# Kernel tuning notes

Measured on AMD Instinct MI355X. Metric: run time of the kernel, lower is better.

## Reference

```python
import jax, jax.numpy as jnp
import numpy as np

CAPACITY = 65536
HIDDEN = 512
NUM_HASHES = 8
HASH_SIZE = 16
BATCH = 2048


def setup_inputs() -> dict:
    key = jax.random.key(0)
    ks = jax.random.split(key, 6)
    scale = 1.0 / np.sqrt(HIDDEN)
    query = jax.random.normal(ks[0], (BATCH, HIDDEN), dtype=jnp.float32)
    memory_keys = jax.random.normal(ks[1], (CAPACITY, HIDDEN), dtype=jnp.float32) * scale
    memory_values = jax.random.normal(ks[2], (CAPACITY, HIDDEN), dtype=jnp.float32) * scale
    hash_projections = jax.random.normal(ks[3], (NUM_HASHES, HIDDEN, HASH_SIZE), dtype=jnp.float32) * scale
    out_w = jax.random.normal(ks[4], (HIDDEN, HIDDEN), dtype=jnp.float32) * scale  # torch Linear weight [out,in]
    out_b = jnp.zeros((HIDDEN,), dtype=jnp.float32)
    return {"query": query, "memory_keys": memory_keys, "memory_values": memory_values,
            "hash_projections": hash_projections, "out_w": out_w, "out_b": out_b, "top_k": 32}


def _compute_hash(x, hash_projections):
    # x: [m, h] -> hash bits [m, num_hashes] in {0,1}
    # einsum 'bh,nhd->bnd' then sum over d then sign-threshold
    proj = jnp.einsum('mh,nhd->mnd', x, hash_projections)
    return (proj.sum(-1) > 0).astype(jnp.int32)


def reference(query, memory_keys, memory_values, hash_projections, out_w, out_b, top_k):
    b, h = query.shape
    q_hash = _compute_hash(query, hash_projections)                    # [b, n]
    k_hash = _compute_hash(memory_keys, hash_projections)              # [c, n] (no_grad in torch)
    # Hamming distance via +/-1 dot product: dot = n - 2*dist (avoids [b,c,n] bool tensor)
    qf = (q_hash * 2 - 1).astype(jnp.float32)
    kf = (k_hash * 2 - 1).astype(jnp.float32)
    dot = jnp.einsum('bn,cn->bc', qf, kf)                              # [b, c]
    hash_dist = ((NUM_HASHES - dot) * 0.5).astype(jnp.int32)           # [b, c]
    k = min(top_k, memory_keys.shape[0])
    _, top_indices = jax.lax.top_k(-hash_dist, k)                      # smallest distances, [b, k]
    selected_keys = memory_keys[top_indices]                           # [b, k, h]
    selected_values = memory_values[top_indices]                       # [b, k, h]
    scores = jnp.einsum('bh,bkh->bk', query, selected_keys) / np.sqrt(h).astype(np.float32)
    attn = jax.nn.softmax(scores, axis=-1)
    memory_output = jnp.einsum('bk,bkh->bh', attn, selected_values)    # [b, h]
    return memory_output @ out_w.T + out_b
```

## Files before the change

kernel.cpp:

```cpp
#include <hip/hip_runtime.h>
#include <stdint.h>

#define BATCH  2048
#define HID    512
#define CAP    65536
#define NHASH  8
#define TOPK   32
#define NSLICE 16
#define SLICE_SZ (CAP / NSLICE)
#define ROWS_TILE 16
#define QTILES (BATCH / ROWS_TILE)
#define KTILES (CAP / ROWS_TILE)
#define TOT_TILES (QTILES + KTILES)
#define HGRID  768

typedef unsigned int   u32;
typedef unsigned long long u64;
typedef double d4 __attribute__((ext_vector_type(4)));

__global__ __launch_bounds__(256) void k_prep(const float* __restrict__ proj,
                                              double* __restrict__ psumT,
                                              u32* __restrict__ hist16,
                                              const float* __restrict__ w,
                                              float* __restrict__ wt) {
    __shared__ float tile[64][65];
    int bi = blockIdx.x, tid = threadIdx.x;
    if (bi < 2) {
        int g = bi * 256 + tid;
        for (int i = g; i < NSLICE * 256; i += 512) hist16[i] = 0;
        int h = g;
        for (int n = 0; n < NHASH; n++) {
            const float* p = proj + ((size_t)n * HID + h) * 16;
            double s = 0.0;
            #pragma unroll
            for (int d = 0; d < 16; d++) s += (double)p[d];
            psumT[(size_t)h * NHASH + n] = s;
        }
    } else {
        int b = bi - 2, bx = b & 7, by = b >> 3;
        int tx = tid & 63, ty = tid >> 6;
        for (int r = ty; r < 64; r += 4)
            tile[r][tx] = w[(size_t)(by * 64 + r) * HID + bx * 64 + tx];
        __syncthreads();
        for (int r = ty; r < 64; r += 4)
            wt[(size_t)(bx * 64 + r) * HID + by * 64 + tx] = tile[tx][r];
    }
}

__global__ __launch_bounds__(256, 3) void k_hash(const float* __restrict__ query,
                                                 const float* __restrict__ keys,
                                                 const double* __restrict__ psumT,
                                                 unsigned char* __restrict__ qhash,
                                                 unsigned char* __restrict__ khash,
                                                 u32* __restrict__ hist16) {
    __shared__ __align__(16) float sX[ROWS_TILE * HID];
    __shared__ double sAcc4[4][ROWS_TILE][8];

    const int tid  = threadIdx.x;
    const int w    = tid >> 6;
    const int m    = (tid & 63) & 15;
    const int kk   = (tid & 63) >> 4;

    d4 z = {0.0, 0.0, 0.0, 0.0};
    d4 pr = __builtin_amdgcn_mfma_f64_16x16x4f64((double)(m + 1), 1.0, z, 0, 0, 0);
    d4 pc = __builtin_amdgcn_mfma_f64_16x16x4f64(1.0, (double)(m + 1), z, 0, 0, 0);
    d4 pp = __builtin_amdgcn_mfma_f64_16x16x4f64((double)(1 << kk),
                                                 (double)(1 << (4 * kk)), z, 0, 0, 0);
    int rowOf[4], colOf[4];
    #pragma unroll
    for (int i = 0; i < 4; i++) {
        rowOf[i] = (int)(pr[i] * 0.25) - 1;
        colOf[i] = (int)(pc[i] * 0.25) - 1;
    }
    u32 pb = (u32)pp[0];
    u32 pairPacked = 0;
    #pragma unroll
    for (int e = 0; e < 16; e++)
        if ((pb >> e) & 1u) pairPacked |= (u32)(e & 3) << (2 * (e >> 2));

    const int kAdj = (int)((pairPacked >> (2 * kk)) & 3u);
    double bfrag[32];
    #pragma unroll
    for (int j = 0; j < 32; j++) {
        int kp = 128 * w + 4 * j + kAdj;
        bfrag[j] = (m < 8) ? psumT[(size_t)kp * NHASH + m] : 0.0;
    }

    const int sw = (m & 7) << 2;

    float4 pf[8];

    {
        int tt = blockIdx.x;
        const float* xb = (tt < QTILES)
            ? (query + (size_t)tt * ROWS_TILE * HID)
            : (keys + (size_t)(tt - QTILES) * ROWS_TILE * HID);
        #pragma unroll
        for (int p = 0; p < 8; p++) {
            int i = tid + 256 * p, r = i >> 7, G = i & 127;
            pf[p] = ((const float4*)(xb + (size_t)r * HID))[G];
        }
        #pragma unroll
        for (int p = 0; p < 8; p++) {
            int i = tid + 256 * p, r = i >> 7, G = i & 127;
            ((float4*)sX)[r * 128 + (G ^ (r & 7))] = pf[p];
        }
        __syncthreads();
    }

    int tt = blockIdx.x;
    for (;;) {
        const int tn = tt + HGRID;
        const bool more = (tn < TOT_TILES);

        if (more) {
            const float* xb = (tn < QTILES)
                ? (query + (size_t)tn * ROWS_TILE * HID)
                : (keys + (size_t)(tn - QTILES) * ROWS_TILE * HID);
            #pragma unroll
            for (int p = 0; p < 8; p++) {
                int i = tid + 256 * p, r = i >> 7, G = i & 127;
                pf[p] = ((const float4*)(xb + (size_t)r * HID))[G];
            }
        }

        d4 ac0 = z, ac1 = z, ac2 = z, ac3 = z;
        const float* sxm = sX + m * HID;
        #pragma unroll
        for (int j8 = 0; j8 < 8; j8++) {
            int k0 = 128 * w + ((4 * j8) ^ sw) + kk;
            ac0 = __builtin_amdgcn_mfma_f64_16x16x4f64((double)sxm[k0],      bfrag[j8],      ac0, 0, 0, 0);
            ac1 = __builtin_amdgcn_mfma_f64_16x16x4f64((double)sxm[k0 + 32], bfrag[j8 + 8],  ac1, 0, 0, 0);
            ac2 = __builtin_amdgcn_mfma_f64_16x16x4f64((double)sxm[k0 + 64], bfrag[j8 + 16], ac2, 0, 0, 0);
            ac3 = __builtin_amdgcn_mfma_f64_16x16x4f64((double)sxm[k0 + 96], bfrag[j8 + 24], ac3, 0, 0, 0);
        }
        d4 acc = (ac0 + ac1) + (ac2 + ac3);

        #pragma unroll
        for (int i = 0; i < 4; i++) {
            if (((unsigned)rowOf[i] < (unsigned)ROWS_TILE) && ((unsigned)colOf[i] < 8u))
                sAcc4[w][rowOf[i]][colOf[i]] = acc[i];
        }
        __syncthreads();

        if (tid < ROWS_TILE) {
            u32 byte = 0;
            #pragma unroll
            for (int n = 0; n < 8; n++) {
                double s = sAcc4[0][tid][n] + sAcc4[1][tid][n]
                         + sAcc4[2][tid][n] + sAcc4[3][tid][n];
                if (s > 0.0) byte |= (1u << n);
            }
            if (tt < QTILES) {
                qhash[tt * ROWS_TILE + tid] = (unsigned char)byte;
            } else {
                int row = (tt - QTILES) * ROWS_TILE + tid;
                khash[row] = (unsigned char)byte;
                atomicAdd(&hist16[(row / SLICE_SZ) * 256 + byte], 1u);
            }
        }
        if (!more) break;

        #pragma unroll
        for (int p = 0; p < 8; p++) {
            int i = tid + 256 * p, r = i >> 7, G = i & 127;
            ((float4*)sX)[r * 128 + (G ^ (r & 7))] = pf[p];
        }
        __syncthreads();
        tt = tn;
    }
}

__global__ __launch_bounds__(256) void k_scan(const u32* __restrict__ hist16,
                                              u32* __restrict__ bucketCnt,
                                              u32* __restrict__ bucketOff,
                                              u32* __restrict__ off16) {
    __shared__ u32 wsum[4];
    int v = threadIdx.x, lane = v & 63, wv = v >> 6;
    u32 tot = 0;
    for (int s = 0; s < NSLICE; s++) tot += hist16[s * 256 + v];
    bucketCnt[v] = tot;
    u32 inc = tot;
    #pragma unroll
    for (int s = 1; s < 64; s <<= 1) {
        u32 n = __shfl_up(inc, s, 64);
        if (lane >= s) inc += n;
    }
    if (lane == 63) wsum[wv] = inc;
    __syncthreads();
    u32 wof = 0;
    for (int i = 0; i < wv; i++) wof += wsum[i];
    u32 base = wof + inc - tot;
    bucketOff[v] = base;
    for (int s = 0; s < NSLICE; s++) { off16[s * 256 + v] = base; base += hist16[s * 256 + v]; }
}

__global__ __launch_bounds__(256) void k_compact(const unsigned char* __restrict__ khash,
                                                 const u32* __restrict__ off16,
                                                 u32* __restrict__ bucketList) {
    __shared__ unsigned char sh[SLICE_SZ];
    int s  = blockIdx.x & (NSLICE - 1);
    int bg = blockIdx.x >> 4;
    ((uint4*)sh)[threadIdx.x] = ((const uint4*)(khash + (size_t)s * SLICE_SZ))[threadIdx.x];
    __syncthreads();
    int w = threadIdx.x >> 6, lane = threadIdx.x & 63;
    int v = bg * 4 + w;
    u32 base = off16[s * 256 + v];
    for (int i = 0; i < SLICE_SZ / 64; i++) {
        int c = i * 64 + lane;
        unsigned char byte = sh[c];
        bool hit = (byte == (unsigned char)v);
        u64 m = __ballot(hit);
        if (hit) {
            int rank = __popcll(m & ((1ull << lane) - 1ull));
            bucketList[base + rank] = (u32)(s * SLICE_SZ + c);
        }
        base += (u32)__popcll(m);
    }
}

__global__ __launch_bounds__(256) void k_attn(const float* __restrict__ keys,
                                              const float* __restrict__ vals,
                                              const float* __restrict__ query,
                                              const unsigned char* __restrict__ qhash,
                                              const u32* __restrict__ bucketCnt,
                                              const u32* __restrict__ bucketOff,
                                              const u32* __restrict__ bucketList,
                                              float* __restrict__ mo) {
    __shared__ int sIdx[TOPK];
    __shared__ float sSc[TOPK], sE[TOPK];
    __shared__ int sPos0;
    int b = blockIdx.x, tid = threadIdx.x;
    int w = tid >> 6, lane = tid & 63;

    if (w == 0) {
        if (lane == 0) sPos0 = 0;
        u32 qh = qhash[b];

        int d[4]; u32 cnt[4], off[4];
        #pragma unroll
        for (int jj = 0; jj < 4; jj++) {
            int v = lane + jj * 64;
            d[jj] = __popc(qh ^ (u32)v);
            cnt[jj] = bucketCnt[v];
            off[jj] = bucketOff[v];
        }

        u32 ct[9];
        #pragma unroll
        for (int t = 0; t < 9; t++) {
            u32 c = 0;
            #pragma unroll
            for (int jj = 0; jj < 4; jj++) c += (d[jj] == t) ? cnt[jj] : 0u;
            #pragma unroll
            for (int s = 32; s >= 1; s >>= 1) c += __shfl_xor(c, s, 64);
            ct[t] = c;
        }

        int dcut = 0; u32 run = 0, before = 0;
        for (int t = 0; t < 9; t++) {
            before = run; run += ct[t];
            if (run >= TOPK) { dcut = t; break; }
        }
        int need = TOPK - (int)before;

        #pragma unroll
        for (int jj = 0; jj < 4; jj++) {
            if (d[jj] < dcut && cnt[jj] > 0) {
                int base = atomicAdd(&sPos0, (int)cnt[jj]);
                for (u32 e = 0; e < cnt[jj]; e++)
                    sIdx[base + e] = (int)bucketList[off[jj] + e];
            }
        }

        int nb = 0;
        #pragma unroll
        for (int jj = 0; jj < 4; jj++) nb += (d[jj] == dcut) ? 1 : 0;
        #pragma unroll
        for (int s = 32; s >= 1; s >>= 1) nb += __shfl_xor(nb, s, 64);

        if (nb == 1) {
            u32 boff = 0xFFFFFFFFu;
            #pragma unroll
            for (int jj = 0; jj < 4; jj++) if (d[jj] == dcut) boff = off[jj];
            #pragma unroll
            for (int s = 32; s >= 1; s >>= 1) boff = min(boff, __shfl_xor(boff, s, 64));
            if (lane < need)
                sIdx[(int)before + lane] = (int)bucketList[boff + lane];
        } else {
            u32 pos[4], end[4]; int val[4];
            #pragma unroll
            for (int jj = 0; jj < 4; jj++) {
                if (d[jj] == dcut && cnt[jj] > 0) {
                    pos[jj] = off[jj]; end[jj] = off[jj] + cnt[jj];
                    val[jj] = (int)bucketList[pos[jj]];
                } else { pos[jj] = 0; end[jj] = 0; val[jj] = 0x7fffffff; }
            }
            for (int it = 0; it < need; it++) {
                int m = min(min(val[0], val[1]), min(val[2], val[3]));
                int g = m;
                #pragma unroll
                for (int s = 32; s >= 1; s >>= 1) g = min(g, __shfl_xor(g, s, 64));
                if (lane == 0) sIdx[(int)before + it] = g;
                if (m == g && g != 0x7fffffff) {
                    #pragma unroll
                    for (int jj = 0; jj < 4; jj++) {
                        if (val[jj] == g) {
                            pos[jj]++;
                            val[jj] = (pos[jj] < end[jj]) ? (int)bucketList[pos[jj]] : 0x7fffffff;
                            break;
                        }
                    }
                }
            }
        }
    }
    __syncthreads();

    const float4* qp = (const float4*)(query + (size_t)b * HID + lane * 8);
    float4 qa = qp[0], qb = qp[1];

    for (int i = w * 8; i < w * 8 + 8; i++) {
        int idx = sIdx[i];
        const float4* kp = (const float4*)(keys + (size_t)idx * HID + lane * 8);
        float4 ka = kp[0], kb = kp[1];
        float dot = qa.x * ka.x + qa.y * ka.y + qa.z * ka.z + qa.w * ka.w
                  + qb.x * kb.x + qb.y * kb.y + qb.z * kb.z + qb.w * kb.w;
        #pragma unroll
        for (int s = 32; s >= 1; s >>= 1) dot += __shfl_xor(dot, s, 64);
        if (lane == 0) sSc[i] = dot * 0.04419417382415922f;
    }
    __syncthreads();

    if (tid < TOPK) {
        float m = -1e30f;
        for (int i = 0; i < TOPK; i++) m = fmaxf(m, sSc[i]);
        sE[tid] = expf(sSc[tid] - m);
    }
    __syncthreads();

    float sum = 0.f;
    for (int i = 0; i < TOPK; i++) sum += sE[i];
    float inv = 1.0f / sum;

    int h0 = tid * 2;
    float a0 = 0.f, a1 = 0.f;
    for (int i = 0; i < TOPK; i++) {
        int idx = sIdx[i];
        float e = sE[i];
        float2 vv = *(const float2*)(vals + (size_t)idx * HID + h0);
        a0 += e * vv.x; a1 += e * vv.y;
    }
    ((float2*)(mo + (size_t)b * HID))[tid] = make_float2(a0 * inv, a1 * inv);
}

__global__ __launch_bounds__(256) void k_proj(const float* __restrict__ mo,
                                              const float* __restrict__ wt,
                                              const float* __restrict__ bias,
                                              float* __restrict__ out) {
    int tid = threadIdx.x;
    int o = (blockIdx.x & 1) * 256 + tid;
    int bb = (blockIdx.x >> 1) * 8;
    float acc[8];
    #pragma unroll
    for (int r = 0; r < 8; r++) acc[r] = 0.f;
    for (int h = 0; h < HID; h++) {
        float wv = wt[(size_t)h * HID + o];
        #pragma unroll
        for (int r = 0; r < 8; r++)
            acc[r] += mo[(size_t)(bb + r) * HID + h] * wv;
    }
    float bv = bias[o];
    #pragma unroll
    for (int r = 0; r < 8; r++)
        out[(size_t)(bb + r) * HID + o] = acc[r] + bv;
}

extern "C" void kernel_launch(void* const* d_in, const int* in_sizes, int n_in,
                              void* d_out, int out_size, void* d_ws, size_t ws_size,
                              hipStream_t stream) {
    const float* query = (const float*)d_in[0];
    const float* keys  = (const float*)d_in[1];
    const float* vals  = (const float*)d_in[2];
    const float* proj  = (const float*)d_in[3];
    const float* outw  = (const float*)d_in[4];
    const float* outbp = (const float*)d_in[5];
    float* out = (float*)d_out;

    char* ws = (char*)d_ws;
    double*        psumT      = (double*)(ws + 0);
    unsigned char* qhash      = (unsigned char*)(ws + 32768);
    unsigned char* khash      = (unsigned char*)(ws + 34816);
    u32*           hist16     = (u32*)(ws + 100352);
    u32*           bucketCnt  = (u32*)(ws + 116736);
    u32*           bucketOff  = (u32*)(ws + 117760);
    u32*           off16      = (u32*)(ws + 118784);
    u32*           bucketList = (u32*)(ws + 135168);
    float*         mo         = (float*)(ws + 397312);
    float*         wt         = (float*)(ws + 4591616);
    (void)in_sizes; (void)n_in; (void)out_size; (void)ws_size;

    k_prep<<<66, 256, 0, stream>>>(proj, psumT, hist16, outw, wt);
    k_hash<<<HGRID, 256, 0, stream>>>(query, keys, psumT, qhash, khash, hist16);
    k_scan<<<1, 256, 0, stream>>>(hist16, bucketCnt, bucketOff, off16);
    k_compact<<<1024, 256, 0, stream>>>(khash, off16, bucketList);
    k_attn<<<BATCH, 256, 0, stream>>>(keys, vals, query, qhash, bucketCnt, bucketOff, bucketList, mo);
    k_proj<<<512, 256, 0, stream>>>(mo, wt, outbp, out);
}
```

Baseline: 390.5 us.

## Double-buffer hash tiles in LDS via direct global-to-LDS loads

The hash kernel now prefetches the next 16-row tile straight into a second LDS buffer with global_load_lds. This replaces the register-staged prefetch and the separate LDS store pass, and the XOR swizzle moves to the global address side. Manual vmcnt/lgkmcnt waits and raw barriers order the ping-pong buffers. In exchange, LDS use doubles, so occupancy drops from 3 to 2 blocks per CU and the persistent grid shrinks from 768 to 512 blocks.

```diff
diff --git a/kernel.cpp b/kernel.cpp
--- a/kernel.cpp
+++ b/kernel.cpp
@@ -12,7 +12,7 @@
 #define QTILES (BATCH / ROWS_TILE)
 #define KTILES (CAP / ROWS_TILE)
 #define TOT_TILES (QTILES + KTILES)
-#define HGRID  768
+#define HGRID  512
 
 typedef unsigned int   u32;
 typedef unsigned long long u64;
@@ -47,19 +47,43 @@
     }
 }
 
-__global__ __launch_bounds__(256, 3) void k_hash(const float* __restrict__ query,
+__device__ __forceinline__ void stage_tile(const float* __restrict__ xb,
+                                           float* buf, int tid) {
+    #pragma unroll
+    for (int p = 0; p < 8; p++) {
+        int i = p * 256 + tid;
+        int r = i >> 7;
+        int G = (i & 127) ^ (r & 7);
+        const float4* g = (const float4*)(xb + (size_t)r * HID) + G;
+        float4* l = ((float4*)buf) + i;
+        __builtin_amdgcn_global_load_lds(
+            (const __attribute__((address_space(1))) void*)g,
+            (__attribute__((address_space(3))) void*)l, 16, 0, 0);
+    }
+}
+
+__global__ __launch_bounds__(256, 2) void k_hash(const float* __restrict__ query,
                                                  const float* __restrict__ keys,
                                                  const double* __restrict__ psumT,
                                                  unsigned char* __restrict__ qhash,
                                                  unsigned char* __restrict__ khash,
                                                  u32* __restrict__ hist16) {
-    __shared__ __align__(16) float sX[ROWS_TILE * HID];
+    __shared__ __align__(16) float sX0[ROWS_TILE * HID];
+    __shared__ __align__(16) float sX1[ROWS_TILE * HID];
     __shared__ double sAcc4[4][ROWS_TILE][8];
 
     const int tid  = threadIdx.x;
     const int w    = tid >> 6;
     const int m    = (tid & 63) & 15;
     const int kk   = (tid & 63) >> 4;
+
+    {
+        int t0 = blockIdx.x;
+        const float* xb = (t0 < QTILES)
+            ? (query + (size_t)t0 * ROWS_TILE * HID)
+            : (keys + (size_t)(t0 - QTILES) * ROWS_TILE * HID);
+        stage_tile(xb, sX0, tid);
+    }
 
     d4 z = {0.0, 0.0, 0.0, 0.0};
     d4 pr = __builtin_amdgcn_mfma_f64_16x16x4f64((double)(m + 1), 1.0, z, 0, 0, 0);
@@ -88,25 +112,8 @@
 
     const int sw = (m & 7) << 2;
 
-    float4 pf[8];
-
-    {
-        int tt = blockIdx.x;
-        const float* xb = (tt < QTILES)
-            ? (query + (size_t)tt * ROWS_TILE * HID)
-            : (keys + (size_t)(tt - QTILES) * ROWS_TILE * HID);
-        #pragma unroll
-        for (int p = 0; p < 8; p++) {
-            int i = tid + 256 * p, r = i >> 7, G = i & 127;
-            pf[p] = ((const float4*)(xb + (size_t)r * HID))[G];
-        }
-        #pragma unroll
-        for (int p = 0; p < 8; p++) {
-            int i = tid + 256 * p, r = i >> 7, G = i & 127;
-            ((float4*)sX)[r * 128 + (G ^ (r & 7))] = pf[p];
-        }
-        __syncthreads();
-    }
+    float* rbuf = sX0;
+    float* wbuf = sX1;
 
     int tt = blockIdx.x;
     for (;;) {
@@ -117,15 +124,16 @@
             const float* xb = (tn < QTILES)
                 ? (query + (size_t)tn * ROWS_TILE * HID)
                 : (keys + (size_t)(tn - QTILES) * ROWS_TILE * HID);
-            #pragma unroll
-            for (int p = 0; p < 8; p++) {
-                int i = tid + 256 * p, r = i >> 7, G = i & 127;
-                pf[p] = ((const float4*)(xb + (size_t)r * HID))[G];
-            }
-        }
+            stage_tile(xb, wbuf, tid);
+            asm volatile("s_waitcnt vmcnt(8)" ::: "memory");
+        } else {
+            asm volatile("s_waitcnt vmcnt(0)" ::: "memory");
+        }
+        __builtin_amdgcn_s_barrier();
+        __builtin_amdgcn_sched_barrier(0);
 
         d4 ac0 = z, ac1 = z, ac2 = z, ac3 = z;
-        const float* sxm = sX + m * HID;
+        const float* sxm = rbuf + m * HID;
         #pragma unroll
         for (int j8 = 0; j8 < 8; j8++) {
             int k0 = 128 * w + ((4 * j8) ^ sw) + kk;
@@ -141,7 +149,9 @@
             if (((unsigned)rowOf[i] < (unsigned)ROWS_TILE) && ((unsigned)colOf[i] < 8u))
                 sAcc4[w][rowOf[i]][colOf[i]] = acc[i];
         }
-        __syncthreads();
+        asm volatile("s_waitcnt lgkmcnt(0)" ::: "memory");
+        __builtin_amdgcn_s_barrier();
+        __builtin_amdgcn_sched_barrier(0);
 
         if (tid < ROWS_TILE) {
             u32 byte = 0;
@@ -161,12 +171,7 @@
         }
         if (!more) break;
 
-        #pragma unroll
-        for (int p = 0; p < 8; p++) {
-            int i = tid + 256 * p, r = i >> 7, G = i & 127;
-            ((float4*)sX)[r * 128 + (G ^ (r & 7))] = pf[p];
-        }
-        __syncthreads();
+        float* t = rbuf; rbuf = wbuf; wbuf = t;
         tt = tn;
     }
 }
```

Result: faster. 357.7 us (-8.4%).
